# Optimization experiments

Measured on AMD Instinct MI355X. Metric: run time of the kernel, lower is better.

Reference implementation:

```python
import jax, jax.numpy as jnp
import numpy as np

B, S, D, H = 2, 2048, 1024, 16
DK = D // H


def setup_inputs() -> dict:
    key = jax.random.key(0)
    ks = jax.random.split(key, 12)
    scale = 1.0 / np.sqrt(D)
    inp = {
        "q": jax.random.normal(ks[0], (B, S, D), dtype=jnp.float32),
        "k": jax.random.normal(ks[1], (B, S, D), dtype=jnp.float32),
        "v": jax.random.normal(ks[2], (B, S, D), dtype=jnp.float32),
        # causal mask, broadcast over batch and heads; 0 -> masked
        "mask": jnp.tril(jnp.ones((S, S), dtype=jnp.int32))[None, None, :, :],
        "wq_w": jax.random.normal(ks[3], (D, D), dtype=jnp.float32) * scale,
        "wq_b": jax.random.normal(ks[4], (D,), dtype=jnp.float32) * scale,
        "wk_w": jax.random.normal(ks[5], (D, D), dtype=jnp.float32) * scale,
        "wk_b": jax.random.normal(ks[6], (D,), dtype=jnp.float32) * scale,
        "wv_w": jax.random.normal(ks[7], (D, D), dtype=jnp.float32) * scale,
        "wv_b": jax.random.normal(ks[8], (D,), dtype=jnp.float32) * scale,
        "wo_w": jax.random.normal(ks[9], (D, D), dtype=jnp.float32) * scale,
        "wo_b": jax.random.normal(ks[10], (D,), dtype=jnp.float32) * scale,
    }
    return inp


def _split_heads(x):
    b, s, _ = x.shape
    return x.reshape(b, s, H, DK).transpose(0, 2, 1, 3)  # [B,H,S,DK]


def reference(q, k, v, mask, wq_w, wq_b, wk_w, wk_b, wv_w, wv_b, wo_w, wo_b):
    Q = _split_heads(q @ wq_w.T + wq_b)
    K = _split_heads(k @ wk_w.T + wk_b)
    V = _split_heads(v @ wv_w.T + wv_b)
    scale = 1.0 / jnp.sqrt(jnp.asarray(DK, dtype=Q.dtype))
    scores = jnp.einsum("bhqd,bhkd->bhqk", Q, K) * scale  # [B,H,S,S]
    scores = jnp.where(mask == 0, jnp.asarray(-1e9, dtype=scores.dtype), scores)
    attn = jax.nn.softmax(scores, axis=-1)
    out = jnp.einsum("bhqk,bhkd->bhqd", attn, V)  # [B,H,S,DK]
    out = out.transpose(0, 2, 1, 3).reshape(out.shape[0], -1, D)  # [B,S,D]
    return out @ wo_w.T + wo_b
```

## Files before the change

kernel.cpp:

```cpp
#include <hip/hip_runtime.h>
#include <hip/hip_bf16.h>

#define B_ 2
#define S_ 2048
#define D_ 1024
#define H_ 16
#define DK_ 64
#define M_ (B_*S_)

typedef __bf16 bf16;
typedef __bf16 bf16x8 __attribute__((ext_vector_type(8)));
typedef __bf16 bf16x4 __attribute__((ext_vector_type(4)));
typedef __bf16 bf16x2 __attribute__((ext_vector_type(2)));
typedef float  f32x4  __attribute__((ext_vector_type(4)));
typedef float  f32x16 __attribute__((ext_vector_type(16)));
typedef int    i32x4  __attribute__((ext_vector_type(4)));

#define GLOAD_LDS16(gp, lp) __builtin_amdgcn_global_load_lds( \
    (const __attribute__((address_space(1))) void*)(gp),      \
    (__attribute__((address_space(3))) void*)(lp), 16, 0, 0)

static __device__ __forceinline__ int packbf(float a, float b) {
  bf16x2 t; t[0] = (bf16)a; t[1] = (bf16)b;
  return __builtin_bit_cast(int, t);
}

__global__ __launch_bounds__(256) void cast_kernel(
    const float* __restrict__ q, const float* __restrict__ k, const float* __restrict__ v,
    const float* __restrict__ wq, const float* __restrict__ wk,
    const float* __restrict__ wv, const float* __restrict__ wo,
    bf16* __restrict__ dst)
{
  const size_t XN = (size_t)M_ * D_;
  const size_t WN = (size_t)D_ * D_;
  size_t e = ((size_t)blockIdx.x * 256 + threadIdx.x) * 8;
  const float* src; size_t off;
  if (e < XN)        { src = q; off = e; }
  else if (e < 2*XN) { src = k; off = e - XN; }
  else if (e < 3*XN) { src = v; off = e - 2*XN; }
  else {
    size_t w = e - 3*XN; size_t wi = w >> 20; off = w & (WN - 1);
    src = (wi == 0) ? wq : (wi == 1) ? wk : (wi == 2) ? wv : wo;
  }
  float4 a = *reinterpret_cast<const float4*>(src + off);
  float4 b = *reinterpret_cast<const float4*>(src + off + 4);
  bf16x8 o;
  o[0]=(bf16)a.x; o[1]=(bf16)a.y; o[2]=(bf16)a.z; o[3]=(bf16)a.w;
  o[4]=(bf16)b.x; o[5]=(bf16)b.y; o[6]=(bf16)b.z; o[7]=(bf16)b.w;
  *reinterpret_cast<bf16x8*>(dst + e) = o;
}

__device__ __forceinline__ void gemm_mainloop_128(
    const bf16* __restrict__ A, const bf16* __restrict__ W,
    int m0, int n0, int Kdim, bf16* As, bf16* Bs, f32x4 acc[4][4])
{
  const int tid  = threadIdx.x;
  const int lane = tid & 63;
  const int wave = tid >> 6;
  const int wr   = wave >> 1;
  const int wc   = wave & 1;
  const int g    = lane >> 4;
  const int c    = lane & 15;

#pragma unroll
  for (int i = 0; i < 4; ++i)
#pragma unroll
    for (int j = 0; j < 4; ++j)
      acc[i][j] = (f32x4){0.f, 0.f, 0.f, 0.f};

  for (int kt = 0; kt < Kdim; kt += 32) {
    __syncthreads();
#pragma unroll
    for (int u = 0; u < 2; ++u) {
      int ch  = tid + u*256;
      int row = ch >> 2;
      int col = (ch & 3) * 8;
      GLOAD_LDS16(A + (size_t)(m0 + row)*Kdim + kt + col, As + ch*8);
      GLOAD_LDS16(W + (size_t)(n0 + row)*Kdim + kt + col, Bs + ch*8);
    }
    __syncthreads();

    bf16x8 af[4], bw[4];
#pragma unroll
    for (int i = 0; i < 4; ++i)
      af[i] = *reinterpret_cast<const bf16x8*>(As + (wr*64 + i*16 + c)*32 + g*8);
#pragma unroll
    for (int j = 0; j < 4; ++j)
      bw[j] = *reinterpret_cast<const bf16x8*>(Bs + (wc*64 + j*16 + c)*32 + g*8);
#pragma unroll
    for (int i = 0; i < 4; ++i)
#pragma unroll
      for (int j = 0; j < 4; ++j)
        acc[i][j] = __builtin_amdgcn_mfma_f32_16x16x32_bf16(af[i], bw[j], acc[i][j], 0, 0, 0);
  }
}

__global__ __launch_bounds__(256) void gemm_qkv_kernel(
    const bf16* __restrict__ X, const bf16* __restrict__ Wb,
    const float* __restrict__ bq, const float* __restrict__ bk, const float* __restrict__ bv,
    bf16* __restrict__ Qo, bf16* __restrict__ Ko, bf16* __restrict__ Vo)
{
  __shared__ bf16 As[128*32];
  __shared__ bf16 Bs[128*32];
  const int z  = blockIdx.z;
  const int m0 = blockIdx.y * 128;
  const int n0 = blockIdx.x * 128;
  const bf16* A = X  + (size_t)z * ((size_t)M_ * D_);
  const bf16* W = Wb + (size_t)z * ((size_t)D_ * D_);
  const float* bias = (z == 0) ? bq : (z == 1) ? bk : bv;
  const float sc = (z == 0) ? 0.18033688011112042f : 1.0f;

  f32x4 acc[4][4];
  gemm_mainloop_128(A, W, m0, n0, D_, As, Bs, acc);

  const int lane = threadIdx.x & 63;
  const int wave = threadIdx.x >> 6;
  const int wr = wave >> 1, wc = wave & 1;
  const int g = lane >> 4,  c = lane & 15;
  bf16* dstQK = (z == 0) ? Qo : Ko;

#pragma unroll
  for (int i = 0; i < 4; ++i) {
#pragma unroll
    for (int j = 0; j < 4; ++j) {
      const int n  = n0 + wc*64 + j*16 + c;
      const float bn = bias[n];
      const int h = n >> 6, dk = n & 63;
      const int mrow = m0 + wr*64 + i*16 + g*4;
      if (z == 2) {
        const int b = mrow >> 11, s = mrow & 2047;
        bf16x4 pv;
#pragma unroll
        for (int r = 0; r < 4; ++r) pv[r] = (bf16)(acc[i][j][r] + bn);
        *reinterpret_cast<bf16x4*>(Vo + ((size_t)((b*H_ + h)*DK_ + dk))*S_ + s) = pv;
      } else {
#pragma unroll
        for (int r = 0; r < 4; ++r) {
          const int m = mrow + r;
          const int b = m >> 11, s = m & 2047;
          dstQK[((size_t)((b*H_ + h)*S_ + s))*DK_ + dk] = (bf16)((acc[i][j][r] + bn) * sc);
        }
      }
    }
  }
}

__global__ __launch_bounds__(256) void gemm_out_kernel(
    const bf16* __restrict__ A, const bf16* __restrict__ W,
    const float* __restrict__ bias, float* __restrict__ out)
{
  __shared__ bf16 As[128*32];
  __shared__ bf16 Bs[128*32];
  const int m0 = blockIdx.y * 128;
  const int n0 = blockIdx.x * 128;

  f32x4 acc[4][4];
  gemm_mainloop_128(A, W, m0, n0, D_, As, Bs, acc);

  const int lane = threadIdx.x & 63;
  const int wave = threadIdx.x >> 6;
  const int wr = wave >> 1, wc = wave & 1;
  const int g = lane >> 4,  c = lane & 15;

#pragma unroll
  for (int i = 0; i < 4; ++i) {
#pragma unroll
    for (int j = 0; j < 4; ++j) {
      const int n = n0 + wc*64 + j*16 + c;
      const float bn = bias[n];
      const int mrow = m0 + wr*64 + i*16 + g*4;
#pragma unroll
      for (int r = 0; r < 4; ++r)
        out[(size_t)(mrow + r)*D_ + n] = acc[i][j][r] + bn;
    }
  }
}

__global__ __launch_bounds__(256, 2) void attn_kernel(
    const bf16* __restrict__ Q, const bf16* __restrict__ K,
    const bf16* __restrict__ Vt, bf16* __restrict__ O)
{
  const int qt   = (int)gridDim.x - 1 - (int)blockIdx.x;
  const int bh   = blockIdx.y;
  const int b    = bh >> 4;
  const int hh   = bh & 15;
  const int q0   = qt * 128;
  const int tid  = threadIdx.x;
  const int wave = tid >> 6;
  const int lane = tid & 63;
  const int ql   = lane & 31;
  const int hi   = lane >> 5;

  const float NEG = -30000.0f;

  __shared__ bf16 Kl[2][64*64];
  __shared__ bf16 Vl[2][64*64];

  const bf16* Qh = Q  + (size_t)bh * (S_*DK_);
  const bf16* Kh = K  + (size_t)bh * (S_*DK_);
  const bf16* Vh = Vt + (size_t)bh * (DK_*S_);

  const int qw0  = q0 + wave*32;
  const int qrow = qw0 + ql;

  bf16x8 qf[4];
#pragma unroll
  for (int ck = 0; ck < 4; ++ck)
    qf[ck] = *reinterpret_cast<const bf16x8*>(Qh + (size_t)qrow*DK_ + ck*16 + hi*8);

  f32x16 o0 = {}, o1 = {};
  float m_ = 0.f, l_ = 0.f;

  const int nt = q0/64 + 2;

#define STAGE_KV(kv0s, bb) do {                                              \
  _Pragma("unroll")                                                          \
  for (int u = 0; u < 2; ++u) {                                              \
    int ch  = tid + u*256;                                                   \
    int row = ch >> 3;                                                       \
    int g   = (ch & 7) ^ (row & 7);            \
    GLOAD_LDS16(Kh + (size_t)((kv0s) + row)*DK_ + g*8, &Kl[bb][ch*8]);       \
    GLOAD_LDS16(Vh + (size_t)row*S_ + (kv0s) + g*8,    &Vl[bb][ch*8]);       \
  }                                                                          \
} while (0)

#define MK_PA(dst, s, base) do {                                               \
    int x0 = packbf(s[(base)+0], s[(base)+1]);                                 \
    int x1 = packbf(s[(base)+2], s[(base)+3]);                                 \
    int y0 = packbf(s[(base)+4], s[(base)+5]);                                 \
    int y1 = packbf(s[(base)+6], s[(base)+7]);                                 \
    int px0 = __shfl_xor(x0, 32), px1 = __shfl_xor(x1, 32);                    \
    int py0 = __shfl_xor(y0, 32), py1 = __shfl_xor(y1, 32);                    \
    i32x4 w;                                                                   \
    w[0] = hi ? py0 : x0;  w[1] = hi ? py1 : x1;                               \
    w[2] = hi ? y0  : px0; w[3] = hi ? y1  : px1;                              \
    dst = __builtin_bit_cast(bf16x8, w);                                       \
  } while (0)

  int cur = 0;
  STAGE_KV(0, 0);
  __syncthreads();

  for (int t = 0; t < nt; ++t) {
    const int kv0 = t * 64;
    if (t + 1 < nt) STAGE_KV((t+1)*64, cur ^ 1);

    if (kv0 <= qw0 + 31) {
      const char* Kb = (const char*)Kl[cur];
      const char* Vb = (const char*)Vl[cur];

      f32x16 st0 = {}, st1 = {};
#pragma unroll
      for (int ck = 0; ck < 4; ++ck) {
        bf16x8 kf0 = *reinterpret_cast<const bf16x8*>(
            Kb + ql*128 + (((ck*2 + hi) ^ (ql & 7)) << 4));
        st0 = __builtin_amdgcn_mfma_f32_32x32x16_bf16(kf0, qf[ck], st0, 0, 0, 0);
        bf16x8 kf1 = *reinterpret_cast<const bf16x8*>(
            Kb + (32 + ql)*128 + (((ck*2 + hi) ^ (ql & 7)) << 4));
        st1 = __builtin_amdgcn_mfma_f32_32x32x16_bf16(kf1, qf[ck], st1, 0, 0, 0);
      }

      if (kv0 + 63 > qw0) {
#pragma unroll
        for (int r = 0; r < 16; ++r) {
          const int kvr = kv0 + (r & 3) + 8*(r >> 2) + 4*hi;
          st0[r] = (kvr      <= qrow) ? st0[r] : NEG;
          st1[r] = (kvr + 32 <= qrow) ? st1[r] : NEG;
        }
      }

      float pm = st0[0];
#pragma unroll
      for (int r = 1; r < 16; ++r) pm = fmaxf(pm, st0[r]);
#pragma unroll
      for (int r = 0; r < 16; ++r) pm = fmaxf(pm, st1[r]);
      pm = fmaxf(pm, __shfl_xor(pm, 32));

      const float mnew = fmaxf(m_, pm);
      const float corr = exp2f(m_ - mnew);
      m_ = mnew;

      float ls = 0.f;
#pragma unroll
      for (int r = 0; r < 16; ++r) {
        float p = exp2f(st0[r] - mnew);
        ls += p;
        st0[r] = p;
      }
#pragma unroll
      for (int r = 0; r < 16; ++r) {
        float p = exp2f(st1[r] - mnew);
        ls += p;
        st1[r] = p;
      }
      l_ = l_ * corr + (ls + __shfl_xor(ls, 32));
      o0 *= corr; o1 *= corr;

      bf16x8 pa[4];
      MK_PA(pa[0], st0, 0);
      MK_PA(pa[1], st0, 8);
      MK_PA(pa[2], st1, 0);
      MK_PA(pa[3], st1, 8);

#pragma unroll
      for (int ck = 0; ck < 4; ++ck) {
        bf16x8 vf0 = *reinterpret_cast<const bf16x8*>(
            Vb + ql*128 + (((ck*2 + hi) ^ (ql & 7)) << 4));
        o0 = __builtin_amdgcn_mfma_f32_32x32x16_bf16(vf0, pa[ck], o0, 0, 0, 0);
        bf16x8 vf1 = *reinterpret_cast<const bf16x8*>(
            Vb + (32 + ql)*128 + (((ck*2 + hi) ^ (ql & 7)) << 4));
        o1 = __builtin_amdgcn_mfma_f32_32x32x16_bf16(vf1, pa[ck], o1, 0, 0, 0);
      }
    }

    __syncthreads();
    cur ^= 1;
  }

  const float linv = 1.0f / l_;
  bf16* orow = O + ((size_t)(b*S_ + qrow)*H_ + hh)*DK_;
#pragma unroll
  for (int w4 = 0; w4 < 4; ++w4) {
    bf16x4 s0, s1;
#pragma unroll
    for (int e = 0; e < 4; ++e) {
      s0[e] = (bf16)(o0[w4*4 + e] * linv);
      s1[e] = (bf16)(o1[w4*4 + e] * linv);
    }
    *reinterpret_cast<bf16x4*>(orow + 8*w4 + 4*hi)      = s0;
    *reinterpret_cast<bf16x4*>(orow + 32 + 8*w4 + 4*hi) = s1;
  }
#undef STAGE_KV
#undef MK_PA
}

extern "C" void kernel_launch(void* const* d_in, const int* in_sizes, int n_in,
                              void* d_out, int out_size, void* d_ws, size_t ws_size,
                              hipStream_t stream)
{
  const float* q    = (const float*)d_in[0];
  const float* k    = (const float*)d_in[1];
  const float* v    = (const float*)d_in[2];
  const float* wq_w = (const float*)d_in[4];
  const float* wq_b = (const float*)d_in[5];
  const float* wk_w = (const float*)d_in[6];
  const float* wk_b = (const float*)d_in[7];
  const float* wv_w = (const float*)d_in[8];
  const float* wv_b = (const float*)d_in[9];
  const float* wo_w = (const float*)d_in[10];
  const float* wo_b = (const float*)d_in[11];

  const size_t XN = (size_t)M_ * D_;
  const size_t WN = (size_t)D_ * D_;
  bf16* ws  = (bf16*)d_ws;
  bf16* xq  = ws;
  bf16* wqb = ws + 3*XN;
  bf16* Qs  = wqb + 4*WN;
  bf16* Ks  = Qs + XN;
  bf16* Vts = Ks + XN;
  bf16* Os  = ws;

  cast_kernel<<<dim3(8192), dim3(256), 0, stream>>>(q, k, v, wq_w, wk_w, wv_w, wo_w, xq);
  gemm_qkv_kernel<<<dim3(8, 32, 3), dim3(256), 0, stream>>>(
      xq, wqb, wq_b, wk_b, wv_b, Qs, Ks, Vts);
  attn_kernel<<<dim3(16, 32), dim3(256), 0, stream>>>(Qs, Ks, Vts, Os);
  gemm_out_kernel<<<dim3(8, 32), dim3(256), 0, stream>>>(Os, wqb + 3*WN, wo_b, (float*)d_out);
}
```

Baseline: 267.7 us.

## Process two Q sub-tiles per wave in attention and shrink output GEMM tiles

The attention kernel now runs 128 threads (2 waves), each wave handling 64 query rows as two 32-row fragments that share every K/V LDS fragment load, which halves LDS read traffic per MFMA. The grid is flattened to 1D and interleaves the heaviest and lightest causal q-tiles to balance load. The output projection GEMM switches to 64x128 tiles with its own main loop, doubling the block count to improve CU occupancy. The trade-off is more register pressure per wave and fewer waves per block to hide latency in attention.

```diff
diff --git a/kernel.cpp b/kernel.cpp
--- a/kernel.cpp
+++ b/kernel.cpp
@@ -149,26 +149,61 @@
     const bf16* __restrict__ A, const bf16* __restrict__ W,
     const float* __restrict__ bias, float* __restrict__ out)
 {
-  __shared__ bf16 As[128*32];
+  __shared__ bf16 As[64*32];
   __shared__ bf16 Bs[128*32];
-  const int m0 = blockIdx.y * 128;
+  const int m0 = blockIdx.y * 64;
   const int n0 = blockIdx.x * 128;
-
-  f32x4 acc[4][4];
-  gemm_mainloop_128(A, W, m0, n0, D_, As, Bs, acc);
-
-  const int lane = threadIdx.x & 63;
-  const int wave = threadIdx.x >> 6;
+  const int tid  = threadIdx.x;
+  const int lane = tid & 63;
+  const int wave = tid >> 6;
   const int wr = wave >> 1, wc = wave & 1;
   const int g = lane >> 4,  c = lane & 15;
 
-#pragma unroll
-  for (int i = 0; i < 4; ++i) {
+  f32x4 acc[2][4];
+#pragma unroll
+  for (int i = 0; i < 2; ++i)
+#pragma unroll
+    for (int j = 0; j < 4; ++j)
+      acc[i][j] = (f32x4){0.f, 0.f, 0.f, 0.f};
+
+  for (int kt = 0; kt < D_; kt += 32) {
+    __syncthreads();
+    {
+      int ch  = tid;
+      int row = ch >> 2;
+      int col = (ch & 3) * 8;
+      GLOAD_LDS16(A + (size_t)(m0 + row)*D_ + kt + col, As + ch*8);
+#pragma unroll
+      for (int u = 0; u < 2; ++u) {
+        int chb  = tid + u*256;
+        int rowb = chb >> 2;
+        int colb = (chb & 3) * 8;
+        GLOAD_LDS16(W + (size_t)(n0 + rowb)*D_ + kt + colb, Bs + chb*8);
+      }
+    }
+    __syncthreads();
+
+    bf16x8 af[2], bw[4];
+#pragma unroll
+    for (int i = 0; i < 2; ++i)
+      af[i] = *reinterpret_cast<const bf16x8*>(As + (wr*32 + i*16 + c)*32 + g*8);
+#pragma unroll
+    for (int j = 0; j < 4; ++j)
+      bw[j] = *reinterpret_cast<const bf16x8*>(Bs + (wc*64 + j*16 + c)*32 + g*8);
+#pragma unroll
+    for (int i = 0; i < 2; ++i)
+#pragma unroll
+      for (int j = 0; j < 4; ++j)
+        acc[i][j] = __builtin_amdgcn_mfma_f32_16x16x32_bf16(af[i], bw[j], acc[i][j], 0, 0, 0);
+  }
+
+#pragma unroll
+  for (int i = 0; i < 2; ++i) {
 #pragma unroll
     for (int j = 0; j < 4; ++j) {
       const int n = n0 + wc*64 + j*16 + c;
       const float bn = bias[n];
-      const int mrow = m0 + wr*64 + i*16 + g*4;
+      const int mrow = m0 + wr*32 + i*16 + g*4;
 #pragma unroll
       for (int r = 0; r < 4; ++r)
         out[(size_t)(mrow + r)*D_ + n] = acc[i][j][r] + bn;
@@ -176,12 +211,13 @@
   }
 }
 
-__global__ __launch_bounds__(256, 2) void attn_kernel(
+__global__ __launch_bounds__(128, 2) void attn_kernel(
     const bf16* __restrict__ Q, const bf16* __restrict__ K,
     const bf16* __restrict__ Vt, bf16* __restrict__ O)
 {
-  const int qt   = (int)gridDim.x - 1 - (int)blockIdx.x;
-  const int bh   = blockIdx.y;
+  const int bx   = blockIdx.x;
+  const int qt   = (bx < 256) ? (15 - (bx >> 5)) : ((bx - 256) >> 5);
+  const int bh   = bx & 31;
   const int b    = bh >> 4;
   const int hh   = bh & 15;
   const int q0   = qt * 128;
@@ -200,23 +236,27 @@
   const bf16* Kh = K  + (size_t)bh * (S_*DK_);
   const bf16* Vh = Vt + (size_t)bh * (DK_*S_);
 
-  const int qw0  = q0 + wave*32;
-  const int qrow = qw0 + ql;
-
-  bf16x8 qf[4];
-#pragma unroll
-  for (int ck = 0; ck < 4; ++ck)
-    qf[ck] = *reinterpret_cast<const bf16x8*>(Qh + (size_t)qrow*DK_ + ck*16 + hi*8);
-
-  f32x16 o0 = {}, o1 = {};
-  float m_ = 0.f, l_ = 0.f;
+  const int qw0 = q0 + wave*64;
+
+  bf16x8 qf[2][4];
+#pragma unroll
+  for (int f = 0; f < 2; ++f)
+#pragma unroll
+    for (int ck = 0; ck < 4; ++ck)
+      qf[f][ck] = *reinterpret_cast<const bf16x8*>(
+          Qh + (size_t)(qw0 + f*32 + ql)*DK_ + ck*16 + hi*8);
+
+  f32x16 o_[2][2];
+#pragma unroll
+  for (int f = 0; f < 2; ++f) { o_[f][0] = (f32x16){}; o_[f][1] = (f32x16){}; }
+  float m_[2] = {0.f, 0.f}, l_[2] = {0.f, 0.f};
 
   const int nt = q0/64 + 2;
 
 #define STAGE_KV(kv0s, bb) do {                                              \
   _Pragma("unroll")                                                          \
-  for (int u = 0; u < 2; ++u) {                                              \
-    int ch  = tid + u*256;                                                   \
+  for (int u = 0; u < 4; ++u) {                                              \
+    int ch  = tid + u*128;               \
     int row = ch >> 3;                                                       \
     int g   = (ch & 7) ^ (row & 7);            \
     GLOAD_LDS16(Kh + (size_t)((kv0s) + row)*DK_ + g*8, &Kl[bb][ch*8]);       \
@@ -245,71 +285,81 @@
     const int kv0 = t * 64;
     if (t + 1 < nt) STAGE_KV((t+1)*64, cur ^ 1);
 
-    if (kv0 <= qw0 + 31) {
+    if (kv0 <= qw0 + 63) {
       const char* Kb = (const char*)Kl[cur];
       const char* Vb = (const char*)Vl[cur];
 
-      f32x16 st0 = {}, st1 = {};
+      f32x16 st[2][2];
+      st[0][0] = (f32x16){}; st[0][1] = (f32x16){};
+      st[1][0] = (f32x16){}; st[1][1] = (f32x16){};
 #pragma unroll
       for (int ck = 0; ck < 4; ++ck) {
-        bf16x8 kf0 = *reinterpret_cast<const bf16x8*>(
-            Kb + ql*128 + (((ck*2 + hi) ^ (ql & 7)) << 4));
-        st0 = __builtin_amdgcn_mfma_f32_32x32x16_bf16(kf0, qf[ck], st0, 0, 0, 0);
-        bf16x8 kf1 = *reinterpret_cast<const bf16x8*>(
-            Kb + (32 + ql)*128 + (((ck*2 + hi) ^ (ql & 7)) << 4));
-        st1 = __builtin_amdgcn_mfma_f32_32x32x16_bf16(kf1, qf[ck], st1, 0, 0, 0);
-      }
-
-      if (kv0 + 63 > qw0) {
+        const int so = ((ck*2 + hi) ^ (ql & 7)) << 4;
+        bf16x8 kf0 = *reinterpret_cast<const bf16x8*>(Kb + ql*128 + so);
+        bf16x8 kf1 = *reinterpret_cast<const bf16x8*>(Kb + (32 + ql)*128 + so);
+#pragma unroll
+        for (int f = 0; f < 2; ++f) {
+          st[f][0] = __builtin_amdgcn_mfma_f32_32x32x16_bf16(kf0, qf[f][ck], st[f][0], 0, 0, 0);
+          st[f][1] = __builtin_amdgcn_mfma_f32_32x32x16_bf16(kf1, qf[f][ck], st[f][1], 0, 0, 0);
+        }
+      }
+
+      bf16x8 pa[2][4];
+#pragma unroll
+      for (int f = 0; f < 2; ++f) {
+        const int qrow = qw0 + f*32 + ql;
+        if (kv0 + 63 > qw0 + f*32) {
+#pragma unroll
+          for (int r = 0; r < 16; ++r) {
+            const int kvr = kv0 + (r & 3) + 8*(r >> 2) + 4*hi;
+            st[f][0][r] = (kvr      <= qrow) ? st[f][0][r] : NEG;
+            st[f][1][r] = (kvr + 32 <= qrow) ? st[f][1][r] : NEG;
+          }
+        }
+
+        float pm = st[f][0][0];
+#pragma unroll
+        for (int r = 1; r < 16; ++r) pm = fmaxf(pm, st[f][0][r]);
+#pragma unroll
+        for (int r = 0; r < 16; ++r) pm = fmaxf(pm, st[f][1][r]);
+        pm = fmaxf(pm, __shfl_xor(pm, 32));
+
+        const float mnew = fmaxf(m_[f], pm);
+        const float corr = exp2f(m_[f] - mnew);
+        m_[f] = mnew;
+
+        float ls = 0.f;
 #pragma unroll
         for (int r = 0; r < 16; ++r) {
-          const int kvr = kv0 + (r & 3) + 8*(r >> 2) + 4*hi;
-          st0[r] = (kvr      <= qrow) ? st0[r] : NEG;
-          st1[r] = (kvr + 32 <= qrow) ? st1[r] : NEG;
-        }
-      }
-
-      float pm = st0[0];
-#pragma unroll
-      for (int r = 1; r < 16; ++r) pm = fmaxf(pm, st0[r]);
-#pragma unroll
-      for (int r = 0; r < 16; ++r) pm = fmaxf(pm, st1[r]);
-      pm = fmaxf(pm, __shfl_xor(pm, 32));
-
-      const float mnew = fmaxf(m_, pm);
-      const float corr = exp2f(m_ - mnew);
-      m_ = mnew;
-
-      float ls = 0.f;
-#pragma unroll
-      for (int r = 0; r < 16; ++r) {
-        float p = exp2f(st0[r] - mnew);
-        ls += p;
-        st0[r] = p;
-      }
-#pragma unroll
-      for (int r = 0; r < 16; ++r) {
-        float p = exp2f(st1[r] - mnew);
-        ls += p;
-        st1[r] = p;
-      }
-      l_ = l_ * corr + (ls + __shfl_xor(ls, 32));
-      o0 *= corr; o1 *= corr;
-
-      bf16x8 pa[4];
-      MK_PA(pa[0], st0, 0);
-      MK_PA(pa[1], st0, 8);
-      MK_PA(pa[2], st1, 0);
-      MK_PA(pa[3], st1, 8);
+          float p = exp2f(st[f][0][r] - mnew);
+          ls += p;
+          st[f][0][r] = p;
+        }
+#pragma unroll
+        for (int r = 0; r < 16; ++r) {
+          float p = exp2f(st[f][1][r] - mnew);
+          ls += p;
+          st[f][1][r] = p;
+        }
+        l_[f] = l_[f] * corr + (ls + __shfl_xor(ls, 32));
+        o_[f][0] *= corr; o_[f][1] *= corr;
+
+        MK_PA(pa[f][0], st[f][0], 0);
+        MK_PA(pa[f][1], st[f][0], 8);
+        MK_PA(pa[f][2], st[f][1], 0);
+        MK_PA(pa[f][3], st[f][1], 8);
+      }
 
 #pragma unroll
       for (int ck = 0; ck < 4; ++ck) {
-        bf16x8 vf0 = *reinterpret_cast<const bf16x8*>(
-            Vb + ql*128 + (((ck*2 + hi) ^ (ql & 7)) << 4));
-        o0 = __builtin_amdgcn_mfma_f32_32x32x16_bf16(vf0, pa[ck], o0, 0, 0, 0);
-        bf16x8 vf1 = *reinterpret_cast<const bf16x8*>(
-            Vb + (32 + ql)*128 + (((ck*2 + hi) ^ (ql & 7)) << 4));
-        o1 = __builtin_amdgcn_mfma_f32_32x32x16_bf16(vf1, pa[ck], o1, 0, 0, 0);
+        const int so = ((ck*2 + hi) ^ (ql & 7)) << 4;
+        bf16x8 vf0 = *reinterpret_cast<const bf16x8*>(Vb + ql*128 + so);
+        bf16x8 vf1 = *reinterpret_cast<const bf16x8*>(Vb + (32 + ql)*128 + so);
+#pragma unroll
+        for (int f = 0; f < 2; ++f) {
+          o_[f][0] = __builtin_amdgcn_mfma_f32_32x32x16_bf16(vf0, pa[f][ck], o_[f][0], 0, 0, 0);
+          o_[f][1] = __builtin_amdgcn_mfma_f32_32x32x16_bf16(vf1, pa[f][ck], o_[f][1], 0, 0, 0);
+        }
       }
     }
 
@@ -317,18 +367,22 @@
     cur ^= 1;
   }
 
-  const float linv = 1.0f / l_;
-  bf16* orow = O + ((size_t)(b*S_ + qrow)*H_ + hh)*DK_;
-#pragma unroll
-  for (int w4 = 0; w4 < 4; ++w4) {
-    bf16x4 s0, s1;
-#pragma unroll
-    for (int e = 0; e < 4; ++e) {
-      s0[e] = (bf16)(o0[w4*4 + e] * linv);
-      s1[e] = (bf16)(o1[w4*4 + e] * linv);
-    }
-    *reinterpret_cast<bf16x4*>(orow + 8*w4 + 4*hi)      = s0;
-    *reinterpret_cast<bf16x4*>(orow + 32 + 8*w4 + 4*hi) = s1;
+#pragma unroll
+  for (int f = 0; f < 2; ++f) {
+    const float linv = 1.0f / l_[f];
+    const int qrow = qw0 + f*32 + ql;
+    bf16* orow = O + ((size_t)(b*S_ + qrow)*H_ + hh)*DK_;
+#pragma unroll
+    for (int w4 = 0; w4 < 4; ++w4) {
+      bf16x4 s0, s1;
+#pragma unroll
+      for (int e = 0; e < 4; ++e) {
+        s0[e] = (bf16)(o_[f][0][w4*4 + e] * linv);
+        s1[e] = (bf16)(o_[f][1][w4*4 + e] * linv);
+      }
+      *reinterpret_cast<bf16x4*>(orow + 8*w4 + 4*hi)      = s0;
+      *reinterpret_cast<bf16x4*>(orow + 32 + 8*w4 + 4*hi) = s1;
+    }
   }
 #undef STAGE_KV
 #undef MK_PA
@@ -363,6 +417,6 @@
   cast_kernel<<<dim3(8192), dim3(256), 0, stream>>>(q, k, v, wq_w, wk_w, wv_w, wo_w, xq);
   gemm_qkv_kernel<<<dim3(8, 32, 3), dim3(256), 0, stream>>>(
       xq, wqb, wq_b, wk_b, wv_b, Qs, Ks, Vts);
-  attn_kernel<<<dim3(16, 32), dim3(256), 0, stream>>>(Qs, Ks, Vts, Os);
-  gemm_out_kernel<<<dim3(8, 32), dim3(256), 0, stream>>>(Os, wqb + 3*WN, wo_b, (float*)d_out);
-}
+  attn_kernel<<<dim3(512), dim3(128), 0, stream>>>(Qs, Ks, Vts, Os);
+  gemm_out_kernel<<<dim3(8, 64), dim3(256), 0, stream>>>(Os, wqb + 3*WN, wo_b, (float*)d_out);
+}
```

Measured after the change: 271.8 us. Within noise of the previous version (+1.5%).
